# Performance work log

Hardware: AMD Instinct MI355X
Metric: run time of the kernel (lower is better)

## Reference

```python
import jax, jax.numpy as jnp
import numpy as np

SR = 22050
N_FFT = 16384
HOP = N_FFT // 2
NF = N_FFT // 2               # 8192 freq bins kept (last rfft bin dropped via [:-1])
H = SR / N_FFT                # uniform FFT-bin spacing in Hz
CENT = (440.0 * 2.0 ** ((np.arange(24, 108, 0.01) - 69.0) / 12.0)).astype(np.float32)  # [8400]
WIN = (0.5 - 0.5 * np.cos(2.0 * np.pi * np.arange(N_FFT) / N_FFT)).astype(np.float32)  # periodic hann

# Data-independent Thomas-algorithm coefficients for the not-a-knot cubic-spline
# tridiagonal system (diag=4, off-diags=1) with M_UNK unknowns (M_2..M_{n-3}).
M_UNK = NF - 4
_cp = np.empty(M_UNK); _inv_den = np.empty(M_UNK)
_inv_den[0] = 0.25; _cp[0] = 0.25
for _i in range(1, M_UNK):
    _inv_den[_i] = 1.0 / (4.0 - _cp[_i - 1])
    _cp[_i] = _inv_den[_i] if _i < M_UNK - 1 else 0.0
CP = jnp.asarray(_cp, jnp.float32)
INV_DEN = jnp.asarray(_inv_den, jnp.float32)
A_LOWER = jnp.asarray(np.where(np.arange(M_UNK) == 0, 0.0, 1.0), jnp.float32)


def _tridiag_solve(rhs):
    # Thomas algorithm with precomputed (data-independent) elimination coeffs.
    def fwd(dprev, xs):
        r, a, inv = xs
        dp = (r - a * dprev) * inv
        return dp, dp
    _, dp = jax.lax.scan(fwd, jnp.float32(0.0), (rhs, A_LOWER, INV_DEN))
    def bwd(xnext, xs):
        d_i, c_i = xs
        x = d_i - c_i * xnext
        return x, x
    _, xs = jax.lax.scan(bwd, jnp.float32(0.0), (dp, CP), reverse=True)
    return xs


def _cubic_interp(y, xq):
    # Not-a-knot cubic spline (scipy interp1d kind='cubic') on uniform grid x_i = i*H.
    h = jnp.float32(H)
    d = (y[:-2] - 2.0 * y[1:-1] + y[2:]) / (h * h)   # second-difference targets d_1..d_{n-2}
    M1, Mn2 = d[0], d[-1]                             # not-a-knot => M_1=d_1, M_{n-2}=d_{n-2}
    rhs = 6.0 * d[1:-1]
    rhs = rhs.at[0].add(-M1).at[-1].add(-Mn2)
    Min = _tridiag_solve(rhs)                         # M_2..M_{n-3}
    M = jnp.concatenate([jnp.stack([2.0 * M1 - Min[0], M1]), Min,
                         jnp.stack([Mn2, 2.0 * Mn2 - Min[-1]])])  # [n] second derivatives
    i = jnp.clip(jnp.floor(xq / h).astype(jnp.int32), 0, y.shape[0] - 2)
    t = xq - i.astype(jnp.float32) * h
    u = h - t
    Mi, Mi1, yi, yi1 = M[i], M[i + 1], y[i], y[i + 1]
    return ((Mi * u ** 3 + Mi1 * t ** 3) / (6.0 * h)
            + (yi - Mi * h * h / 6.0) * u / h
            + (yi1 - Mi1 * h * h / 6.0) * t / h)


def _tuning_scores(audio, w_smooth, w_detect):
    # torchaudio Spectrogram: center reflect-pad, periodic hann, power=2
    x = jnp.pad(audio, N_FFT // 2, mode='reflect')
    T = 1 + (x.shape[0] - N_FFT) // HOP
    idx = jnp.arange(T)[:, None] * HOP + jnp.arange(N_FFT)[None, :]
    frames = x[idx] * jnp.asarray(WIN)                 # [T, n_fft]
    spec = jnp.abs(jnp.fft.rfft(frames, axis=1)) ** 2  # [T, n_fft//2+1]
    fft_spec = jnp.log(100.0 * spec + 1.0).sum(0)[:NF] # sum over time, drop Nyquist bin
    cent = _cubic_interp(fft_spec, jnp.asarray(CENT))  # [8400]
    smoothed = jnp.convolve(cent, w_smooth, mode='same')
    filtered = jax.nn.relu(cent - smoothed)
    scores = jax.lax.conv_general_dilated(
        filtered[None, None, :], w_detect[None, None, :],
        window_strides=(1,), padding=[(50, 50)], rhs_dilation=(100,))[0, 0, :100]
    return scores


def setup_inputs():
    key = jax.random.key(0)
    audio = jax.random.normal(key, (16777216,), dtype=jnp.float32)
    w_smooth = jnp.ones((101,), jnp.float32) / 101.0   # mean filter, as in module init
    w_detect = jnp.ones((84,), jnp.float32)            # all-ones detector kernel
    return {"audio": audio, "w_smooth": w_smooth, "w_detect": w_detect}


def reference(audio, w_smooth, w_detect):
    scores = _tuning_scores(audio, w_smooth, w_detect)
    detuning = (jnp.argmax(scores) - 50).astype(jnp.int32)
    return detuning, scores
```

## Files before the change

### kernel.cpp

```cpp
#include <hip/hip_runtime.h>
#include <math.h>

#define NBINS   8192
#define L_AUDIO 16777216
#define T_FRAMES 2049
#define NQ      8400
#define MUNK    8188

__device__ __forceinline__ int refl_idx(int m) {
    if (m < 0) m = -m;
    if (m >= L_AUDIO) m = 2 * L_AUDIO - 2 - m;
    return m;
}
__device__ __forceinline__ float2 cmul(float2 a, float2 b) {
    return make_float2(fmaf(a.x, b.x, -a.y * b.y), fmaf(a.x, b.y, a.y * b.x));
}
__device__ __forceinline__ float2 csq(float2 a) {
    return make_float2(fmaf(a.x, a.x, -a.y * a.y), 2.0f * a.x * a.y);
}
__device__ __forceinline__ void r4(float2& x0, float2& x1, float2& x2, float2& x3,
                                   float2 w1, float2 w2, float2 w3) {
    float2 t0 = make_float2(x0.x + x2.x, x0.y + x2.y);
    float2 t1 = make_float2(x1.x + x3.x, x1.y + x3.y);
    float2 t2 = make_float2(x0.x - x2.x, x0.y - x2.y);
    float2 t3 = make_float2(x1.x - x3.x, x1.y - x3.y);
    float2 b1 = make_float2(t2.x + t3.y, t2.y - t3.x);
    float2 b3 = make_float2(t2.x - t3.y, t2.y + t3.x);
    x0 = make_float2(t0.x + t1.x, t0.y + t1.y);
    x1 = cmul(w1, b1);
    x2 = cmul(w2, make_float2(t0.x - t1.x, t0.y - t1.y));
    x3 = cmul(w3, b3);
}
__device__ __forceinline__ void r8(float2 x[8], float2 w) {
    const float c = 0.70710678118654752f;
    float2 w2 = csq(w), w3 = cmul(w, w2), w4 = csq(w2);
    r4(x[0], x[2], x[4], x[6], w, w2, w3);
    float2 wE   = make_float2(c * (w.x + w.y),  c * (w.y - w.x));
    float2 w2E2 = make_float2(w2.y, -w2.x);
    float2 w3E3 = make_float2(c * (w3.y - w3.x), -c * (w3.x + w3.y));
    r4(x[1], x[3], x[5], x[7], wE, w2E2, w3E3);
#pragma unroll
    for (int r = 0; r < 4; ++r) {
        float2 a = x[2 * r], b = x[2 * r + 1];
        x[2 * r]     = make_float2(a.x + b.x, a.y + b.y);
        float2 d     = make_float2(a.x - b.x, a.y - b.y);
        x[2 * r + 1] = cmul(w4, d);
    }
}

__global__ __launch_bounds__(512, 2) void fft_pow_kernel(
        const float* __restrict__ audio, float* __restrict__ partial, int P) {
    __shared__ float2 buf[8718];
    const int t = threadIdx.x;

    const int phit  = t + (t >> 4);
    const int q2    = t & 127;
    const int base2 = 1090 * (t >> 7) + q2 + (q2 >> 4);
    const int base3 = 136 * (t >> 4) + ((t >> 4) >> 2) + (t & 15);
    const int base4 = 17 * t + (t >> 5);
    const int tp    = (512 - t) & 511;
    const int PBt = (t & 3) * 2048 + ((t >> 2) & 1) * 1024 + ((t >> 3) & 3) * 256
                  + ((t >> 5) & 1) * 128 + ((t >> 6) & 3) * 32 + ((t >> 8) & 1) * 16;
    const int PBp = (tp & 3) * 2048 + ((tp >> 2) & 1) * 1024 + ((tp >> 3) & 3) * 256
                  + ((tp >> 5) & 1) * 128 + ((tp >> 6) & 3) * 32 + ((tp >> 8) & 1) * 16;
    const int ubA = PBt + (PBt >> 4) + (PBt >> 9);
    const int ubB = PBp + (PBp >> 4) + (PBp >> 9);

    const float2 ONE = make_float2(1.0f, 0.0f);
    const float2 K8  = make_float2(0.92387953251128674f, -0.38268343236508977f);
    const float2 KD  = make_float2(0.99999992646574f, -0.00038349518757f);
    float2 wU  = make_float2(cospif((float)t * (1.0f / 8192.0f)),
                             -sinpif((float)t * (1.0f / 8192.0f)));
    float2 w1  = csq(wU);
    float2 wodd = cmul(w1, KD);
    float2 w2t = make_float2(cospif((float)q2 * (1.0f / 512.0f)),
                             -sinpif((float)q2 * (1.0f / 512.0f)));
    float2 w3t = make_float2(cospif((float)(t & 15) * (1.0f / 64.0f)),
                             -sinpif((float)(t & 15) * (1.0f / 64.0f)));
    const float K16c[16] = {1.0f, 0.98078528040323044f, 0.92387953251128674f,
        0.83146961230254524f, 0.70710678118654752f, 0.55557023301960222f,
        0.38268343236508977f, 0.19509032201612825f, 0.0f, -0.19509032201612825f,
        -0.38268343236508977f, -0.55557023301960222f, -0.70710678118654752f,
        -0.83146961230254524f, -0.92387953251128674f, -0.98078528040323044f};
    const float K16s[16] = {0.0f, -0.19509032201612825f, -0.38268343236508977f,
        -0.55557023301960222f, -0.70710678118654752f, -0.83146961230254524f,
        -0.92387953251128674f, -0.98078528040323044f, -1.0f, -0.98078528040323044f,
        -0.92387953251128674f, -0.83146961230254524f, -0.70710678118654752f,
        -0.55557023301960222f, -0.38268343236508977f, -0.19509032201612825f};
    const float W16C[16] = {1.0f, 0.92387953251128674f, 0.70710678118654752f,
        0.38268343236508977f, 0.0f, -0.38268343236508977f, -0.70710678118654752f,
        -0.92387953251128674f, -1.0f, -0.92387953251128674f, -0.70710678118654752f,
        -0.38268343236508977f, 0.0f, 0.38268343236508977f, 0.70710678118654752f,
        0.92387953251128674f};
    const float W16S[16] = {0.0f, 0.38268343236508977f, 0.70710678118654752f,
        0.92387953251128674f, 1.0f, 0.92387953251128674f, 0.70710678118654752f,
        0.38268343236508977f, 0.0f, -0.38268343236508977f, -0.70710678118654752f,
        -0.92387953251128674f, -1.0f, -0.92387953251128674f, -0.70710678118654752f,
        -0.38268343236508977f};

    float acc[16];
#pragma unroll
    for (int u = 0; u < 16; ++u) acc[u] = 0.0f;

    for (int f = blockIdx.x; f < T_FRAMES; f += P) {
        __syncthreads();
        const bool interior = (f != 0) && (f != T_FRAMES - 1);
        const float2* au2 = (const float2*)audio + 4096 * (f - 1);
        const int baseS = f * 8192 - 8192;
#pragma unroll 1
        for (int g = 0; g < 2; ++g) {
            float2 x[8];
            if (interior) {
#pragma unroll
                for (int j = 0; j < 8; ++j) {
                    int idx = t + 512 * g + 1024 * j;
                    float2 p = au2[idx];
                    const int uix = g + 2 * j;
                    float c0 = 0.5f - 0.5f * (w1.x * W16C[uix] + w1.y * W16S[uix]);
                    float c1 = 0.5f - 0.5f * (wodd.x * W16C[uix] + wodd.y * W16S[uix]);
                    x[j] = make_float2(p.x * c0, p.y * c1);
                }
            } else {
#pragma unroll
                for (int j = 0; j < 8; ++j) {
                    int idx = t + 512 * g + 1024 * j;
                    float a0 = audio[refl_idx(baseS + 2 * idx)];
                    float a1 = audio[refl_idx(baseS + 2 * idx + 1)];
                    const int uix = g + 2 * j;
                    float c0 = 0.5f - 0.5f * (w1.x * W16C[uix] + w1.y * W16S[uix]);
                    float c1 = 0.5f - 0.5f * (wodd.x * W16C[uix] + wodd.y * W16S[uix]);
                    x[j] = make_float2(a0 * c0, a1 * c1);
                }
            }
            float2 w = g ? cmul(w1, K8) : w1;
            r8(x, w);
#pragma unroll
            for (int j = 0; j < 8; ++j) buf[phit + 545 * g + 1090 * j] = x[j];
        }
        __syncthreads();
#pragma unroll 1
        for (int g = 0; g < 2; ++g) {
            float2 x[8];
            const int bs = base2 + 4360 * g;
#pragma unroll
            for (int j = 0; j < 8; ++j) x[j] = buf[bs + 136 * j + (j >> 2)];
            r8(x, w2t);
#pragma unroll
            for (int j = 0; j < 8; ++j) buf[bs + 136 * j + (j >> 2)] = x[j];
        }
        __syncthreads();
#pragma unroll 1
        for (int g = 0; g < 2; ++g) {
            float2 x[8];
            const int bs = base3 + 4360 * g;
#pragma unroll
            for (int j = 0; j < 8; ++j) x[j] = buf[bs + 17 * j];
            r8(x, w3t);
#pragma unroll
            for (int j = 0; j < 8; ++j) buf[bs + 17 * j] = x[j];
        }
        __syncthreads();
        {
            float2 a[8], x[8];
#pragma unroll
            for (int j = 0; j < 8; ++j) a[j] = buf[base4 + 2 * j];
            r8(a, ONE);
#pragma unroll
            for (int j = 0; j < 8; ++j) x[j] = buf[base4 + 1 + 2 * j];
            r8(x, K8);
#pragma unroll
            for (int j = 0; j < 8; ++j) {
                buf[base4 + 2 * j]     = make_float2(a[j].x + x[j].x, a[j].y + x[j].y);
                buf[base4 + 2 * j + 1] = make_float2(a[j].x - x[j].x, a[j].y - x[j].y);
            }
        }
        __syncthreads();
#pragma unroll
        for (int u = 0; u < 16; ++u) {
            const int off = (u & 3) * 4 + ((u >> 2) & 1) * 2 + (u >> 3);
            int u2 = t ? (15 - u) : ((16 - u) & 15);
            int off2 = (u2 & 3) * 4 + ((u2 >> 2) & 1) * 2 + (u2 >> 3);
            float2 A = buf[ubA + off];
            float2 B = buf[ubB + off2];
            float Xer = 0.5f * (A.x + B.x);
            float Xei = 0.5f * (A.y - B.y);
            float Xor = 0.5f * (A.y + B.y);
            float Xoi = -0.5f * (A.x - B.x);
            float2 w = cmul(wU, make_float2(K16c[u], K16s[u]));
            float Xr = Xer + Xor * w.x - Xoi * w.y;
            float Xi = Xei + Xor * w.y + Xoi * w.x;
            float pw = Xr * Xr + Xi * Xi;
            acc[u] += __logf(fmaf(100.0f, pw, 1.0f));
        }
    }
#pragma unroll
    for (int u = 0; u < 16; ++u)
        partial[(size_t)blockIdx.x * NBINS + t + 512 * u] = acc[u];
}

__global__ __launch_bounds__(256) void reduce_kernel(
        const float* __restrict__ partial, float* __restrict__ spec, int P) {
    __shared__ float s[4][65];
    const int bin0 = blockIdx.x * 64;
    const int bo = threadIdx.x & 63;
    const int g  = threadIdx.x >> 6;
    const int rows = P >> 2;
    float a0 = 0.f, a1 = 0.f;
    int r = 0;
    const float* base = partial + (size_t)g * rows * NBINS + bin0 + bo;
    for (; r + 2 <= rows; r += 2) {
        a0 += base[(size_t)r * NBINS];
        a1 += base[(size_t)(r + 1) * NBINS];
    }
    for (; r < rows; ++r) a0 += base[(size_t)r * NBINS];
    s[g][bo] = a0 + a1;
    __syncthreads();
    if (threadIdx.x < 64)
        spec[bin0 + threadIdx.x] = (s[0][threadIdx.x] + s[1][threadIdx.x])
                                 + (s[2][threadIdx.x] + s[3][threadIdx.x]);
}

__global__ __launch_bounds__(256) void cent_spline_kernel(
        const float* __restrict__ spec, const float* __restrict__ wsm,
        float* __restrict__ filt) {
    __shared__ float ys[768];
    __shared__ float dps[704];
    __shared__ float Ms[640];
    __shared__ float cs[356];
    __shared__ float wsm_s[101];
    __shared__ float invden_s[64];
    const int tid = threadIdx.x;
    const int j0 = blockIdx.x * 256;
    const float h = 22050.0f / 16384.0f;
    const float hh = h * h;

    if (tid == 0) {
        double v = 0.25;
        invden_s[0] = 0.25f;
        for (int i = 1; i < 64; ++i) { v = 1.0 / (4.0 - v); invden_s[i] = (float)v; }
    }
    for (int r = tid; r < 101; r += 256) wsm_s[r] = wsm[r];

    const int jLo = max(j0 - 50, 0);
    const int jHi = min(j0 + 305, NQ - 1);
    const float xqLo = (float)(440.0 * exp2(((double)jLo * 0.01 - 45.0) * (1.0 / 12.0)));
    const float xqHi = (float)(440.0 * exp2(((double)jHi * 0.01 - 45.0) * (1.0 / 12.0)));
    const int iLo = min(max((int)floorf(xqLo / h), 0), 8190);
    const int iHi = min(max((int)floorf(xqHi / h), 0), 8190);
    const int pLo = max(iLo - 2, 0);
    const int pHi = min(iHi - 1, MUNK - 1);
    const int bHi = min(pHi + 64, MUNK - 1);
    const int yLo = max(pLo - 64, 0);
    const int yHi = bHi + 3;
    const int ny  = yHi - yLo + 1;

    for (int k = tid; k < ny; k += 256) ys[k] = spec[yLo + k];
    __syncthreads();
    const float cst = invden_s[63];

    {
        const int nch = (bHi - pLo + 32) >> 5;
        if (tid < nch) {
            const int s = pLo + (tid << 5);
            const int e = min(s + 31, bHi);
            const int ws = max(s - 64, 0);
            float dprev = 0.0f;
            for (int i = ws; i <= e; ++i) {
                float d1 = (ys[i + 1 - yLo] - 2.0f * ys[i + 2 - yLo]
                            + ys[i + 3 - yLo]) / hh;
                float r = 6.0f * d1;
                if (i == 0) r -= (ys[0] - 2.0f * ys[1] + ys[2]) / hh;
                float val = (i == 0) ? r : (r - dprev);
                float dpv = val * ((i < 64) ? invden_s[i] : cst);
                if (i >= s) dps[i - pLo] = dpv;
                dprev = dpv;
            }
        }
    }
    __syncthreads();
    {
        const int nch = (pHi - pLo + 32) >> 5;
        if (tid < nch) {
            const int s = pLo + (tid << 5);
            const int e = min(s + 31, pHi);
            const int ws2 = min(e + 64, bHi);
            float xnext = 0.0f;
            for (int i = ws2; i >= s; --i) {
                float cp = (i == MUNK - 1) ? 0.0f : ((i < 64) ? invden_s[i] : cst);
                float xv = dps[i - pLo] - cp * xnext;
                if (i <= e) Ms[2 + i - iLo] = xv;
                xnext = xv;
            }
        }
    }
    __syncthreads();
    for (int r = tid; r < 356; r += 256) {
        int j = j0 - 50 + r;
        float v = 0.0f;
        if (j >= 0 && j < NQ) {
            double e = ((double)j * 0.01 - 45.0) * (1.0 / 12.0);
            float xq = (float)(440.0 * exp2(e));
            int i = min(max((int)floorf(xq / h), 0), 8190);
            float tt = xq - (float)i * h;
            float uu = h - tt;
            float Mi = Ms[i - iLo], Mi1 = Ms[i + 1 - iLo];
            float yi = ys[i - yLo], yi1 = ys[i + 1 - yLo];
            v = (Mi * uu * uu * uu + Mi1 * tt * tt * tt) / (6.0f * h)
              + (yi - Mi * hh / 6.0f) * uu / h
              + (yi1 - Mi1 * hh / 6.0f) * tt / h;
        }
        cs[r] = v;
    }
    __syncthreads();
    int j = j0 + tid;
    if (j < NQ) {
        float s = 0.0f;
        for (int m = 0; m < 101; ++m) s = fmaf(wsm_s[m], cs[tid + 100 - m], s);
        float fv = cs[tid + 50] - s;
        filt[j] = fv > 0.0f ? fv : 0.0f;
    }
}

__global__ __launch_bounds__(256) void comb_argmax_kernel(
        const float* __restrict__ filt, const float* __restrict__ wdet,
        float* __restrict__ out) {
    __shared__ float fs[NQ];
    __shared__ float wd[84];
    __shared__ float sc[100];
    const int t = threadIdx.x;
    for (int k = t; k < NQ; k += 256) fs[k] = filt[k];
    if (t < 84) wd[t] = wdet[t];
    __syncthreads();
    if (t < 100) {
        float s = 0.0f;
        for (int k = 0; k < 84; ++k) {
            int ix = t - 50 + 100 * k;
            if (ix >= 0) s = fmaf(wd[k], fs[ix], s);
        }
        sc[t] = s;
        out[1 + t] = s;
    }
    __syncthreads();
    if (t < 64) {
        float v = (t < 100) ? sc[t] : -1e30f;
        int i = t;
        int t2 = t + 64;
        float v2 = (t2 < 100) ? sc[t2] : -1e30f;
        if (v2 > v) { v = v2; i = t2; }
#pragma unroll
        for (int off = 32; off; off >>= 1) {
            float ov = __shfl_xor(v, off, 64);
            int   oi = __shfl_xor(i, off, 64);
            if (ov > v || (ov == v && oi < i)) { v = ov; i = oi; }
        }
        if (t == 0) out[0] = (float)(i - 50);
    }
}

extern "C" void kernel_launch(void* const* d_in, const int* in_sizes, int n_in,
                              void* d_out, int out_size, void* d_ws, size_t ws_size,
                              hipStream_t stream) {
    const float* audio = (const float*)d_in[0];
    const float* wsm   = (const float*)d_in[1];
    const float* wdet  = (const float*)d_in[2];
    float* out = (float*)d_out;
    float* ws  = (float*)d_ws;

    long cap = (long)(ws_size / sizeof(float) / NBINS) - 1;
    int P = (int)(cap < 4 ? 4 : (cap > 512 ? 512 : cap));
    P &= ~3;
    float* spec    = ws;
    float* partial = ws + NBINS;
    float* filt    = ws + 2 * NBINS;

    hipLaunchKernelGGL(fft_pow_kernel, dim3(P), dim3(512), 0, stream,
                       audio, partial, P);
    hipLaunchKernelGGL(reduce_kernel, dim3(128), dim3(256), 0, stream,
                       partial, spec, P);
    hipLaunchKernelGGL(cent_spline_kernel, dim3(33), dim3(256), 0, stream,
                       spec, wsm, filt);
    hipLaunchKernelGGL(comb_argmax_kernel, dim3(1), dim3(256), 0, stream,
                       filt, wdet, out);
}
```

Before: 124.0 us.

## Prefetch next frame's audio into registers and unroll FFT stage groups

Loads the next frame's 16 audio samples per thread into registers before the final spectrum accumulation stage, so global memory latency overlaps with the current frame's post-processing and log-power work. It also fully unrolls the two-group loops in the first three radix-8 stages and issues all shared-memory loads before the butterflies, exposing more instruction-level parallelism. The cost is higher register pressure (16 extra float2 held across the loop), which may lower occupancy.

```diff
diff --git a/kernel.cpp b/kernel.cpp
--- a/kernel.cpp
+++ b/kernel.cpp
@@ -102,71 +102,92 @@
 #pragma unroll
     for (int u = 0; u < 16; ++u) acc[u] = 0.0f;
 
+    float2 ld[16];
+    auto preload = [&](int f) {
+        if (f >= T_FRAMES) return;
+        const bool interior = (f != 0) && (f != T_FRAMES - 1);
+        if (interior) {
+            const float2* au2 = (const float2*)audio + 4096 * (f - 1);
+#pragma unroll
+            for (int j = 0; j < 8; ++j) {
+                ld[j]     = au2[t + 1024 * j];
+                ld[8 + j] = au2[t + 512 + 1024 * j];
+            }
+        } else {
+            const int baseS = f * 8192 - 8192;
+#pragma unroll
+            for (int j = 0; j < 8; ++j) {
+                int i0 = baseS + 2 * (t + 1024 * j);
+                int i1 = baseS + 2 * (t + 512 + 1024 * j);
+                ld[j]     = make_float2(audio[refl_idx(i0)], audio[refl_idx(i0 + 1)]);
+                ld[8 + j] = make_float2(audio[refl_idx(i1)], audio[refl_idx(i1 + 1)]);
+            }
+        }
+    };
+    preload(blockIdx.x);
+
     for (int f = blockIdx.x; f < T_FRAMES; f += P) {
         __syncthreads();
-        const bool interior = (f != 0) && (f != T_FRAMES - 1);
-        const float2* au2 = (const float2*)audio + 4096 * (f - 1);
-        const int baseS = f * 8192 - 8192;
-#pragma unroll 1
-        for (int g = 0; g < 2; ++g) {
-            float2 x[8];
-            if (interior) {
-#pragma unroll
-                for (int j = 0; j < 8; ++j) {
-                    int idx = t + 512 * g + 1024 * j;
-                    float2 p = au2[idx];
-                    const int uix = g + 2 * j;
-                    float c0 = 0.5f - 0.5f * (w1.x * W16C[uix] + w1.y * W16S[uix]);
-                    float c1 = 0.5f - 0.5f * (wodd.x * W16C[uix] + wodd.y * W16S[uix]);
-                    x[j] = make_float2(p.x * c0, p.y * c1);
-                }
-            } else {
-#pragma unroll
-                for (int j = 0; j < 8; ++j) {
-                    int idx = t + 512 * g + 1024 * j;
-                    float a0 = audio[refl_idx(baseS + 2 * idx)];
-                    float a1 = audio[refl_idx(baseS + 2 * idx + 1)];
-                    const int uix = g + 2 * j;
-                    float c0 = 0.5f - 0.5f * (w1.x * W16C[uix] + w1.y * W16S[uix]);
-                    float c1 = 0.5f - 0.5f * (wodd.x * W16C[uix] + wodd.y * W16S[uix]);
-                    x[j] = make_float2(a0 * c0, a1 * c1);
-                }
-            }
-            float2 w = g ? cmul(w1, K8) : w1;
-            r8(x, w);
-#pragma unroll
-            for (int j = 0; j < 8; ++j) buf[phit + 545 * g + 1090 * j] = x[j];
+        {
+            float2 y[8];
+#pragma unroll
+            for (int j = 0; j < 8; ++j) {
+                const int uix = 2 * j;
+                float c0 = 0.5f - 0.5f * (w1.x * W16C[uix] + w1.y * W16S[uix]);
+                float c1 = 0.5f - 0.5f * (wodd.x * W16C[uix] + wodd.y * W16S[uix]);
+                y[j] = make_float2(ld[j].x * c0, ld[j].y * c1);
+            }
+            r8(y, w1);
+#pragma unroll
+            for (int j = 0; j < 8; ++j) buf[phit + 1090 * j] = y[j];
+            float2 z[8];
+#pragma unroll
+            for (int j = 0; j < 8; ++j) {
+                const int uix = 2 * j + 1;
+                float c0 = 0.5f - 0.5f * (w1.x * W16C[uix] + w1.y * W16S[uix]);
+                float c1 = 0.5f - 0.5f * (wodd.x * W16C[uix] + wodd.y * W16S[uix]);
+                z[j] = make_float2(ld[8 + j].x * c0, ld[8 + j].y * c1);
+            }
+            r8(z, cmul(w1, K8));
+#pragma unroll
+            for (int j = 0; j < 8; ++j) buf[phit + 545 + 1090 * j] = z[j];
         }
         __syncthreads();
-#pragma unroll 1
-        for (int g = 0; g < 2; ++g) {
-            float2 x[8];
-            const int bs = base2 + 4360 * g;
-#pragma unroll
-            for (int j = 0; j < 8; ++j) x[j] = buf[bs + 136 * j + (j >> 2)];
-            r8(x, w2t);
-#pragma unroll
-            for (int j = 0; j < 8; ++j) buf[bs + 136 * j + (j >> 2)] = x[j];
+        {
+            float2 x0[8], x1[8];
+#pragma unroll
+            for (int j = 0; j < 8; ++j) x0[j] = buf[base2 + 136 * j + (j >> 2)];
+#pragma unroll
+            for (int j = 0; j < 8; ++j) x1[j] = buf[base2 + 4360 + 136 * j + (j >> 2)];
+            r8(x0, w2t);
+#pragma unroll
+            for (int j = 0; j < 8; ++j) buf[base2 + 136 * j + (j >> 2)] = x0[j];
+            r8(x1, w2t);
+#pragma unroll
+            for (int j = 0; j < 8; ++j) buf[base2 + 4360 + 136 * j + (j >> 2)] = x1[j];
         }
         __syncthreads();
-#pragma unroll 1
-        for (int g = 0; g < 2; ++g) {
-            float2 x[8];
-            const int bs = base3 + 4360 * g;
-#pragma unroll
-            for (int j = 0; j < 8; ++j) x[j] = buf[bs + 17 * j];
-            r8(x, w3t);
-#pragma unroll
-            for (int j = 0; j < 8; ++j) buf[bs + 17 * j] = x[j];
+        {
+            float2 x0[8], x1[8];
+#pragma unroll
+            for (int j = 0; j < 8; ++j) x0[j] = buf[base3 + 17 * j];
+#pragma unroll
+            for (int j = 0; j < 8; ++j) x1[j] = buf[base3 + 4360 + 17 * j];
+            r8(x0, w3t);
+#pragma unroll
+            for (int j = 0; j < 8; ++j) buf[base3 + 17 * j] = x0[j];
+            r8(x1, w3t);
+#pragma unroll
+            for (int j = 0; j < 8; ++j) buf[base3 + 4360 + 17 * j] = x1[j];
         }
         __syncthreads();
         {
             float2 a[8], x[8];
 #pragma unroll
             for (int j = 0; j < 8; ++j) a[j] = buf[base4 + 2 * j];
+#pragma unroll
+            for (int j = 0; j < 8; ++j) x[j] = buf[base4 + 1 + 2 * j];
             r8(a, ONE);
-#pragma unroll
-            for (int j = 0; j < 8; ++j) x[j] = buf[base4 + 1 + 2 * j];
             r8(x, K8);
 #pragma unroll
             for (int j = 0; j < 8; ++j) {
@@ -174,6 +195,7 @@
                 buf[base4 + 2 * j + 1] = make_float2(a[j].x - x[j].x, a[j].y - x[j].y);
             }
         }
+        preload(f + P);
         __syncthreads();
 #pragma unroll
         for (int u = 0; u < 16; ++u) {
```

After: 202.2 us. 63.1% more time.

## Fuse reduce, spline and comb stages into one kernel with atomic grid barriers

Applied to the files above, without the earlier changes.

Merges the three post-FFT kernels into a single 128-block kernel. Blocks synchronise through an atomic counter spin-wait after the partial-sum reduction, and a last-block-done counter hands off the comb/argmax stage. Counters live in unused spec slots (indices 8188/8189) and are zeroed by the FFT kernel; spec bins 8188+ are no longer written. This removes two kernel launch gaps, at the cost of a spin-wait that assumes all 128 blocks are co-resident.

```diff
diff --git a/kernel.cpp b/kernel.cpp
--- a/kernel.cpp
+++ b/kernel.cpp
@@ -52,6 +52,11 @@
         const float* __restrict__ audio, float* __restrict__ partial, int P) {
     __shared__ float2 buf[8718];
     const int t = threadIdx.x;
+
+    if (blockIdx.x == 0 && t == 0) {
+        unsigned int* cz = (unsigned int*)(partial - 4);
+        cz[0] = 0u; cz[1] = 0u;
+    }
 
     const int phit  = t + (t >> 4);
     const int q2    = t & 127;
@@ -198,162 +203,192 @@
         partial[(size_t)blockIdx.x * NBINS + t + 512 * u] = acc[u];
 }
 
-__global__ __launch_bounds__(256) void reduce_kernel(
-        const float* __restrict__ partial, float* __restrict__ spec, int P) {
-    __shared__ float s[4][65];
-    const int bin0 = blockIdx.x * 64;
-    const int bo = threadIdx.x & 63;
-    const int g  = threadIdx.x >> 6;
-    const int rows = P >> 2;
-    float a0 = 0.f, a1 = 0.f;
-    int r = 0;
-    const float* base = partial + (size_t)g * rows * NBINS + bin0 + bo;
-    for (; r + 2 <= rows; r += 2) {
-        a0 += base[(size_t)r * NBINS];
-        a1 += base[(size_t)(r + 1) * NBINS];
-    }
-    for (; r < rows; ++r) a0 += base[(size_t)r * NBINS];
-    s[g][bo] = a0 + a1;
+__global__ __launch_bounds__(256) void fused_post_kernel(
+        float* __restrict__ ws, const float* __restrict__ wsm,
+        const float* __restrict__ wdet, float* __restrict__ out, int P) {
+    float* spec    = ws;
+    float* partial = ws + NBINS;
+    float* filt    = ws + 2 * NBINS;
+    unsigned int* c0 = (unsigned int*)(ws + 8188);
+    unsigned int* c1 = (unsigned int*)(ws + 8189);
+    const int tid = threadIdx.x;
+    const int bid = blockIdx.x;
+
+    {
+        __shared__ float sred[4][65];
+        const int bin0 = bid * 64;
+        const int bo = tid & 63;
+        const int g  = tid >> 6;
+        const int rows = P >> 2;
+        float a0 = 0.f, a1 = 0.f;
+        int r = 0;
+        const float* base = partial + (size_t)g * rows * NBINS + bin0 + bo;
+        for (; r + 2 <= rows; r += 2) {
+            a0 += base[(size_t)r * NBINS];
+            a1 += base[(size_t)(r + 1) * NBINS];
+        }
+        for (; r < rows; ++r) a0 += base[(size_t)r * NBINS];
+        sred[g][bo] = a0 + a1;
+        __syncthreads();
+        if (tid < 64) {
+            int bin = bin0 + tid;
+            if (bin < 8188)
+                spec[bin] = (sred[0][tid] + sred[1][tid])
+                          + (sred[2][tid] + sred[3][tid]);
+        }
+        __syncthreads();
+    }
+    __threadfence();
+    if (tid == 0)
+        __hip_atomic_fetch_add(c0, 1u, __ATOMIC_RELEASE, __HIP_MEMORY_SCOPE_AGENT);
+    if (bid >= 33) return;
+    if (tid == 0) {
+        while (__hip_atomic_load(c0, __ATOMIC_ACQUIRE, __HIP_MEMORY_SCOPE_AGENT) < 128u) {}
+    }
     __syncthreads();
-    if (threadIdx.x < 64)
-        spec[bin0 + threadIdx.x] = (s[0][threadIdx.x] + s[1][threadIdx.x])
-                                 + (s[2][threadIdx.x] + s[3][threadIdx.x]);
-}
-
-__global__ __launch_bounds__(256) void cent_spline_kernel(
-        const float* __restrict__ spec, const float* __restrict__ wsm,
-        float* __restrict__ filt) {
-    __shared__ float ys[768];
-    __shared__ float dps[704];
-    __shared__ float Ms[640];
-    __shared__ float cs[356];
-    __shared__ float wsm_s[101];
-    __shared__ float invden_s[64];
-    const int tid = threadIdx.x;
-    const int j0 = blockIdx.x * 256;
-    const float h = 22050.0f / 16384.0f;
-    const float hh = h * h;
-
+    __threadfence();
+
+    {
+        __shared__ float ys[768];
+        __shared__ float dps[704];
+        __shared__ float Ms[640];
+        __shared__ float cs[356];
+        __shared__ float wsm_s[101];
+        __shared__ float invden_s[64];
+        const int j0 = bid * 256;
+        const float h = 22050.0f / 16384.0f;
+        const float hh = h * h;
+
+        if (tid == 0) {
+            double v = 0.25;
+            invden_s[0] = 0.25f;
+            for (int i = 1; i < 64; ++i) { v = 1.0 / (4.0 - v); invden_s[i] = (float)v; }
+        }
+        for (int r = tid; r < 101; r += 256) wsm_s[r] = wsm[r];
+
+        const int jLo = max(j0 - 50, 0);
+        const int jHi = min(j0 + 305, NQ - 1);
+        const float xqLo = (float)(440.0 * exp2(((double)jLo * 0.01 - 45.0) * (1.0 / 12.0)));
+        const float xqHi = (float)(440.0 * exp2(((double)jHi * 0.01 - 45.0) * (1.0 / 12.0)));
+        const int iLo = min(max((int)floorf(xqLo / h), 0), 8190);
+        const int iHi = min(max((int)floorf(xqHi / h), 0), 8190);
+        const int pLo = max(iLo - 2, 0);
+        const int pHi = min(iHi - 1, MUNK - 1);
+        const int bHi = min(pHi + 64, MUNK - 1);
+        const int yLo = max(pLo - 64, 0);
+        const int yHi = bHi + 3;
+        const int ny  = yHi - yLo + 1;
+
+        for (int k = tid; k < ny; k += 256) ys[k] = spec[yLo + k];
+        __syncthreads();
+        const float cst = invden_s[63];
+
+        {
+            const int nch = (bHi - pLo + 32) >> 5;
+            if (tid < nch) {
+                const int s = pLo + (tid << 5);
+                const int e = min(s + 31, bHi);
+                const int wstart = max(s - 64, 0);
+                float dprev = 0.0f;
+                for (int i = wstart; i <= e; ++i) {
+                    float d1 = (ys[i + 1 - yLo] - 2.0f * ys[i + 2 - yLo]
+                                + ys[i + 3 - yLo]) / hh;
+                    float r = 6.0f * d1;
+                    if (i == 0) r -= (ys[0] - 2.0f * ys[1] + ys[2]) / hh;
+                    float val = (i == 0) ? r : (r - dprev);
+                    float dpv = val * ((i < 64) ? invden_s[i] : cst);
+                    if (i >= s) dps[i - pLo] = dpv;
+                    dprev = dpv;
+                }
+            }
+        }
+        __syncthreads();
+        {
+            const int nch = (pHi - pLo + 32) >> 5;
+            if (tid < nch) {
+                const int s = pLo + (tid << 5);
+                const int e = min(s + 31, pHi);
+                const int ws2 = min(e + 64, bHi);
+                float xnext = 0.0f;
+                for (int i = ws2; i >= s; --i) {
+                    float cp = (i == MUNK - 1) ? 0.0f : ((i < 64) ? invden_s[i] : cst);
+                    float xv = dps[i - pLo] - cp * xnext;
+                    if (i <= e) Ms[2 + i - iLo] = xv;
+                    xnext = xv;
+                }
+            }
+        }
+        __syncthreads();
+        for (int r = tid; r < 356; r += 256) {
+            int j = j0 - 50 + r;
+            float v = 0.0f;
+            if (j >= 0 && j < NQ) {
+                double e = ((double)j * 0.01 - 45.0) * (1.0 / 12.0);
+                float xq = (float)(440.0 * exp2(e));
+                int i = min(max((int)floorf(xq / h), 0), 8190);
+                float tt = xq - (float)i * h;
+                float uu = h - tt;
+                float Mi = Ms[i - iLo], Mi1 = Ms[i + 1 - iLo];
+                float yi = ys[i - yLo], yi1 = ys[i + 1 - yLo];
+                v = (Mi * uu * uu * uu + Mi1 * tt * tt * tt) / (6.0f * h)
+                  + (yi - Mi * hh / 6.0f) * uu / h
+                  + (yi1 - Mi1 * hh / 6.0f) * tt / h;
+            }
+            cs[r] = v;
+        }
+        __syncthreads();
+        int j = j0 + tid;
+        if (j < NQ) {
+            float s = 0.0f;
+            for (int m = 0; m < 101; ++m) s = fmaf(wsm_s[m], cs[tid + 100 - m], s);
+            float fv = cs[tid + 50] - s;
+            filt[j] = fv > 0.0f ? fv : 0.0f;
+        }
+        __syncthreads();
+    }
+    __shared__ unsigned int lastflag;
+    __threadfence();
     if (tid == 0) {
-        double v = 0.25;
-        invden_s[0] = 0.25f;
-        for (int i = 1; i < 64; ++i) { v = 1.0 / (4.0 - v); invden_s[i] = (float)v; }
-    }
-    for (int r = tid; r < 101; r += 256) wsm_s[r] = wsm[r];
-
-    const int jLo = max(j0 - 50, 0);
-    const int jHi = min(j0 + 305, NQ - 1);
-    const float xqLo = (float)(440.0 * exp2(((double)jLo * 0.01 - 45.0) * (1.0 / 12.0)));
-    const float xqHi = (float)(440.0 * exp2(((double)jHi * 0.01 - 45.0) * (1.0 / 12.0)));
-    const int iLo = min(max((int)floorf(xqLo / h), 0), 8190);
-    const int iHi = min(max((int)floorf(xqHi / h), 0), 8190);
-    const int pLo = max(iLo - 2, 0);
-    const int pHi = min(iHi - 1, MUNK - 1);
-    const int bHi = min(pHi + 64, MUNK - 1);
-    const int yLo = max(pLo - 64, 0);
-    const int yHi = bHi + 3;
-    const int ny  = yHi - yLo + 1;
-
-    for (int k = tid; k < ny; k += 256) ys[k] = spec[yLo + k];
+        unsigned int prev =
+            __hip_atomic_fetch_add(c1, 1u, __ATOMIC_ACQ_REL, __HIP_MEMORY_SCOPE_AGENT);
+        lastflag = (prev == 32u) ? 1u : 0u;
+    }
     __syncthreads();
-    const float cst = invden_s[63];
+    if (!lastflag) return;
+    __threadfence();
 
     {
-        const int nch = (bHi - pLo + 32) >> 5;
-        if (tid < nch) {
-            const int s = pLo + (tid << 5);
-            const int e = min(s + 31, bHi);
-            const int ws = max(s - 64, 0);
-            float dprev = 0.0f;
-            for (int i = ws; i <= e; ++i) {
-                float d1 = (ys[i + 1 - yLo] - 2.0f * ys[i + 2 - yLo]
-                            + ys[i + 3 - yLo]) / hh;
-                float r = 6.0f * d1;
-                if (i == 0) r -= (ys[0] - 2.0f * ys[1] + ys[2]) / hh;
-                float val = (i == 0) ? r : (r - dprev);
-                float dpv = val * ((i < 64) ? invden_s[i] : cst);
-                if (i >= s) dps[i - pLo] = dpv;
-                dprev = dpv;
-            }
-        }
-    }
-    __syncthreads();
-    {
-        const int nch = (pHi - pLo + 32) >> 5;
-        if (tid < nch) {
-            const int s = pLo + (tid << 5);
-            const int e = min(s + 31, pHi);
-            const int ws2 = min(e + 64, bHi);
-            float xnext = 0.0f;
-            for (int i = ws2; i >= s; --i) {
-                float cp = (i == MUNK - 1) ? 0.0f : ((i < 64) ? invden_s[i] : cst);
-                float xv = dps[i - pLo] - cp * xnext;
-                if (i <= e) Ms[2 + i - iLo] = xv;
-                xnext = xv;
-            }
-        }
-    }
-    __syncthreads();
-    for (int r = tid; r < 356; r += 256) {
-        int j = j0 - 50 + r;
-        float v = 0.0f;
-        if (j >= 0 && j < NQ) {
-            double e = ((double)j * 0.01 - 45.0) * (1.0 / 12.0);
-            float xq = (float)(440.0 * exp2(e));
-            int i = min(max((int)floorf(xq / h), 0), 8190);
-            float tt = xq - (float)i * h;
-            float uu = h - tt;
-            float Mi = Ms[i - iLo], Mi1 = Ms[i + 1 - iLo];
-            float yi = ys[i - yLo], yi1 = ys[i + 1 - yLo];
-            v = (Mi * uu * uu * uu + Mi1 * tt * tt * tt) / (6.0f * h)
-              + (yi - Mi * hh / 6.0f) * uu / h
-              + (yi1 - Mi1 * hh / 6.0f) * tt / h;
-        }
-        cs[r] = v;
-    }
-    __syncthreads();
-    int j = j0 + tid;
-    if (j < NQ) {
-        float s = 0.0f;
-        for (int m = 0; m < 101; ++m) s = fmaf(wsm_s[m], cs[tid + 100 - m], s);
-        float fv = cs[tid + 50] - s;
-        filt[j] = fv > 0.0f ? fv : 0.0f;
-    }
-}
-
-__global__ __launch_bounds__(256) void comb_argmax_kernel(
-        const float* __restrict__ filt, const float* __restrict__ wdet,
-        float* __restrict__ out) {
-    __shared__ float fs[NQ];
-    __shared__ float wd[84];
-    __shared__ float sc[100];
-    const int t = threadIdx.x;
-    for (int k = t; k < NQ; k += 256) fs[k] = filt[k];
-    if (t < 84) wd[t] = wdet[t];
-    __syncthreads();
-    if (t < 100) {
-        float s = 0.0f;
-        for (int k = 0; k < 84; ++k) {
-            int ix = t - 50 + 100 * k;
-            if (ix >= 0) s = fmaf(wd[k], fs[ix], s);
-        }
-        sc[t] = s;
-        out[1 + t] = s;
-    }
-    __syncthreads();
-    if (t < 64) {
-        float v = (t < 100) ? sc[t] : -1e30f;
-        int i = t;
-        int t2 = t + 64;
-        float v2 = (t2 < 100) ? sc[t2] : -1e30f;
-        if (v2 > v) { v = v2; i = t2; }
-#pragma unroll
-        for (int off = 32; off; off >>= 1) {
-            float ov = __shfl_xor(v, off, 64);
-            int   oi = __shfl_xor(i, off, 64);
-            if (ov > v || (ov == v && oi < i)) { v = ov; i = oi; }
-        }
-        if (t == 0) out[0] = (float)(i - 50);
+        __shared__ float fs[NQ];
+        __shared__ float wd[84];
+        __shared__ float sc[100];
+        const int t = tid;
+        for (int k = t; k < NQ; k += 256) fs[k] = filt[k];
+        if (t < 84) wd[t] = wdet[t];
+        __syncthreads();
+        if (t < 100) {
+            float s = 0.0f;
+            for (int k = 0; k < 84; ++k) {
+                int ix = t - 50 + 100 * k;
+                if (ix >= 0) s = fmaf(wd[k], fs[ix], s);
+            }
+            sc[t] = s;
+            out[1 + t] = s;
+        }
+        __syncthreads();
+        if (t < 64) {
+            float v = (t < 100) ? sc[t] : -1e30f;
+            int i = t;
+            int t2 = t + 64;
+            float v2 = (t2 < 100) ? sc[t2] : -1e30f;
+            if (v2 > v) { v = v2; i = t2; }
+#pragma unroll
+            for (int off = 32; off; off >>= 1) {
+                float ov = __shfl_xor(v, off, 64);
+                int   oi = __shfl_xor(i, off, 64);
+                if (ov > v || (ov == v && oi < i)) { v = ov; i = oi; }
+            }
+            if (t == 0) out[0] = (float)(i - 50);
+        }
     }
 }
 
@@ -369,16 +404,10 @@
     long cap = (long)(ws_size / sizeof(float) / NBINS) - 1;
     int P = (int)(cap < 4 ? 4 : (cap > 512 ? 512 : cap));
     P &= ~3;
-    float* spec    = ws;
     float* partial = ws + NBINS;
-    float* filt    = ws + 2 * NBINS;
 
     hipLaunchKernelGGL(fft_pow_kernel, dim3(P), dim3(512), 0, stream,
                        audio, partial, P);
-    hipLaunchKernelGGL(reduce_kernel, dim3(128), dim3(256), 0, stream,
-                       partial, spec, P);
-    hipLaunchKernelGGL(cent_spline_kernel, dim3(33), dim3(256), 0, stream,
-                       spec, wsm, filt);
-    hipLaunchKernelGGL(comb_argmax_kernel, dim3(1), dim3(256), 0, stream,
-                       filt, wdet, out);
-}
+    hipLaunchKernelGGL(fused_post_kernel, dim3(128), dim3(256), 0, stream,
+                       ws, wsm, wdet, out, P);
+}
```

Measured after the change: 136.2 us. +9.9%, slower.

## Rebalance tail frame onto last block and vectorize partial reduction

Applied to the files above, without the earlier changes.

The FFT kernel now gives the leftover frame 2048 (the 2049th frame) to the last block only, by jumping that block's loop index to it, so no other block runs an extra iteration and the tail wave is shorter. The reduction kernel uses float4 loads, unrolls 16 rows per step, and runs with fewer, narrower blocks. The aim is to cut the load-imbalance tail in the main kernel and the memory latency of the partial-sum reduction. The frame-remapping logic depends on P and the loop-index tweak is subtle, so there is a risk of skipped or double-counted frames for some P values.

```diff
diff --git a/kernel.cpp b/kernel.cpp
--- a/kernel.cpp
+++ b/kernel.cpp
@@ -103,6 +103,7 @@
     for (int u = 0; u < 16; ++u) acc[u] = 0.0f;
 
     for (int f = blockIdx.x; f < T_FRAMES; f += P) {
+        if (f == 2048 && (int)blockIdx.x != P - 1) break;
         __syncthreads();
         const bool interior = (f != 0) && (f != T_FRAMES - 1);
         const float2* au2 = (const float2*)audio + 4096 * (f - 1);
@@ -192,32 +193,56 @@
             float pw = Xr * Xr + Xi * Xi;
             acc[u] += __logf(fmaf(100.0f, pw, 1.0f));
         }
+        if (f < 2048 && f + P >= 2048 && (int)blockIdx.x == P - 1) f = 2048 - P;
     }
 #pragma unroll
     for (int u = 0; u < 16; ++u)
         partial[(size_t)blockIdx.x * NBINS + t + 512 * u] = acc[u];
 }
 
-__global__ __launch_bounds__(256) void reduce_kernel(
+__global__ __launch_bounds__(128) void reduce_kernel(
         const float* __restrict__ partial, float* __restrict__ spec, int P) {
-    __shared__ float s[4][65];
-    const int bin0 = blockIdx.x * 64;
-    const int bo = threadIdx.x & 63;
-    const int g  = threadIdx.x >> 6;
+    __shared__ float4 s[4][33];
+    const int bin0 = blockIdx.x * 128;
+    const int co = threadIdx.x & 31;
+    const int g  = threadIdx.x >> 5;
     const int rows = P >> 2;
-    float a0 = 0.f, a1 = 0.f;
+    const int RS = NBINS / 4;
+    const float4* base = (const float4*)(partial + (size_t)g * rows * NBINS + bin0) + co;
+    float4 a0 = make_float4(0.f, 0.f, 0.f, 0.f);
+    float4 a1 = make_float4(0.f, 0.f, 0.f, 0.f);
     int r = 0;
-    const float* base = partial + (size_t)g * rows * NBINS + bin0 + bo;
+    for (; r + 16 <= rows; r += 16) {
+        float4 l[16];
+#pragma unroll
+        for (int q = 0; q < 16; ++q) l[q] = base[(size_t)(r + q) * RS];
+#pragma unroll
+        for (int q = 0; q < 16; q += 2) {
+            a0.x += l[q].x; a0.y += l[q].y; a0.z += l[q].z; a0.w += l[q].w;
+            a1.x += l[q+1].x; a1.y += l[q+1].y; a1.z += l[q+1].z; a1.w += l[q+1].w;
+        }
+    }
     for (; r + 2 <= rows; r += 2) {
-        a0 += base[(size_t)r * NBINS];
-        a1 += base[(size_t)(r + 1) * NBINS];
-    }
-    for (; r < rows; ++r) a0 += base[(size_t)r * NBINS];
-    s[g][bo] = a0 + a1;
-    __syncthreads();
-    if (threadIdx.x < 64)
-        spec[bin0 + threadIdx.x] = (s[0][threadIdx.x] + s[1][threadIdx.x])
-                                 + (s[2][threadIdx.x] + s[3][threadIdx.x]);
+        float4 l0 = base[(size_t)r * RS];
+        float4 l1 = base[(size_t)(r + 1) * RS];
+        a0.x += l0.x; a0.y += l0.y; a0.z += l0.z; a0.w += l0.w;
+        a1.x += l1.x; a1.y += l1.y; a1.z += l1.z; a1.w += l1.w;
+    }
+    for (; r < rows; ++r) {
+        float4 l0 = base[(size_t)r * RS];
+        a0.x += l0.x; a0.y += l0.y; a0.z += l0.z; a0.w += l0.w;
+    }
+    s[g][co] = make_float4(a0.x + a1.x, a0.y + a1.y, a0.z + a1.z, a0.w + a1.w);
+    __syncthreads();
+    if (threadIdx.x < 32) {
+        float4 s0 = s[0][threadIdx.x], s1 = s[1][threadIdx.x];
+        float4 s2 = s[2][threadIdx.x], s3 = s[3][threadIdx.x];
+        float4 v = make_float4((s0.x + s1.x) + (s2.x + s3.x),
+                               (s0.y + s1.y) + (s2.y + s3.y),
+                               (s0.z + s1.z) + (s2.z + s3.z),
+                               (s0.w + s1.w) + (s2.w + s3.w));
+        ((float4*)(spec + bin0))[threadIdx.x] = v;
+    }
 }
 
 __global__ __launch_bounds__(256) void cent_spline_kernel(
@@ -375,7 +400,7 @@
 
     hipLaunchKernelGGL(fft_pow_kernel, dim3(P), dim3(512), 0, stream,
                        audio, partial, P);
-    hipLaunchKernelGGL(reduce_kernel, dim3(128), dim3(256), 0, stream,
+    hipLaunchKernelGGL(reduce_kernel, dim3(64), dim3(128), 0, stream,
                        partial, spec, P);
     hipLaunchKernelGGL(cent_spline_kernel, dim3(33), dim3(256), 0, stream,
                        spec, wsm, filt);
```

Measured after the change: 114.7 us. 1.08x faster.
